# Kernel tuning notes

Measured on AMD Instinct MI355X. Metric: run time of the kernel, lower is better.

## Reference

```python
import jax, jax.numpy as jnp
import numpy as np

B, K, D = 8, 1024, 512
H, DQ, DV = 8, 64, 64


def setup_inputs() -> dict:
    key = jax.random.key(0)
    ks = jax.random.split(key, 11)
    s = 0.02  # param init scale
    return {
        "query": jax.random.normal(ks[0], (B, K, D), jnp.float32),
        "key": jax.random.normal(ks[1], (B, K, D), jnp.float32),
        "value": jax.random.normal(ks[2], (B, K, D), jnp.float32),
        "Wq": jax.random.normal(ks[3], (D, H * DQ), jnp.float32) * s,
        "bq": jax.random.normal(ks[4], (H * DQ,), jnp.float32) * s,
        "Wk": jax.random.normal(ks[5], (D, H * DQ), jnp.float32) * s,
        "bk": jax.random.normal(ks[6], (H * DQ,), jnp.float32) * s,
        "Wv": jax.random.normal(ks[7], (D, H * DV), jnp.float32) * s,
        "bv": jax.random.normal(ks[8], (H * DV,), jnp.float32) * s,
        "Wo": jax.random.normal(ks[9], (H * DV, D), jnp.float32) * s,
        "bo": jax.random.normal(ks[10], (D,), jnp.float32) * s,
    }


def reference(query, key, value, Wq, bq, Wk, bk, Wv, bv, Wo, bo):
    b, k, _ = query.shape
    # Linear projections, split into heads: chunk(h, dim=-1) + cat(dim=0)
    # is equivalent to reshape (b, k, h, d) with head on a separate axis.
    q = (query @ Wq + bq).reshape(b, k, H, DQ)  # b k h dq
    kk = (key @ Wk + bk).reshape(b, k, H, DQ)   # b k h dq
    v = (value @ Wv + bv).reshape(b, k, H, DV)  # b k h dv
    # NOTE: original scales by sqrt(K) (sequence length), not sqrt(dq).
    scale = 1.0 / jnp.sqrt(jnp.asarray(k, q.dtype))
    scores = jnp.einsum("bqhd,bkhd->bhqk", q, kk) * scale
    attn = jax.nn.softmax(scores, axis=-1)
    ctx = jnp.einsum("bhqk,bkhd->bqhd", attn, v).reshape(b, k, H * DV)
    return ctx @ Wo + bo
```

## Files before the change

### kernel.cpp

```cpp
#include <hip/hip_runtime.h>
#include <hip/hip_bf16.h>

#define DEVI __device__ __forceinline__

typedef __attribute__((ext_vector_type(4))) float f32x4;
typedef __attribute__((ext_vector_type(8))) short bf16x8;

static constexpr int BB  = 8;
static constexpr int SEQ = 1024;
static constexpr int DIM = 512;
static constexpr int NH  = 8;
static constexpr int HD  = 64;
static constexpr int M   = BB * SEQ;


DEVI unsigned short f2bf(float x) {
  unsigned int u = __builtin_bit_cast(unsigned int, x);
  u += 0x7fffu + ((u >> 16) & 1u);
  return (unsigned short)(u >> 16);
}

DEVI float fexp2(float x) {
#if __has_builtin(__builtin_amdgcn_exp2f)
  return __builtin_amdgcn_exp2f(x);
#else
  float r; asm("v_exp_f32 %0, %1" : "=v"(r) : "v"(x)); return r;
#endif
}

DEVI void gload_lds16(const unsigned short* g, unsigned short* l) {
  __builtin_amdgcn_global_load_lds(
      (const __attribute__((address_space(1))) void*)g,
      (__attribute__((address_space(3))) void*)l, 16, 0, 0);
}


__global__ __launch_bounds__(256) void cvt3_kernel(const float* __restrict__ a,
                                                   const float* __restrict__ b,
                                                   const float* __restrict__ c,
                                                   unsigned short* __restrict__ oa,
                                                   unsigned short* __restrict__ ob,
                                                   unsigned short* __restrict__ oc) {
  const float* in = (blockIdx.y == 0) ? a : ((blockIdx.y == 1) ? b : c);
  unsigned short* out = (blockIdx.y == 0) ? oa : ((blockIdx.y == 1) ? ob : oc);
  int i = (blockIdx.x * 256 + threadIdx.x) * 4;
  float4 v = *reinterpret_cast<const float4*>(in + i);
  ushort4 o;
  o.x = f2bf(v.x); o.y = f2bf(v.y); o.z = f2bf(v.z); o.w = f2bf(v.w);
  *reinterpret_cast<ushort4*>(out + i) = o;
}


__global__ __launch_bounds__(256) void cvt_t4_kernel(const float* __restrict__ w0,
                                                     const float* __restrict__ w1,
                                                     const float* __restrict__ w2,
                                                     const float* __restrict__ w3,
                                                     unsigned short* __restrict__ o0,
                                                     unsigned short* __restrict__ o1,
                                                     unsigned short* __restrict__ o2,
                                                     unsigned short* __restrict__ o3) {
  const float* in = (blockIdx.z == 0) ? w0 : ((blockIdx.z == 1) ? w1 : ((blockIdx.z == 2) ? w2 : w3));
  unsigned short* out = (blockIdx.z == 0) ? o0 : ((blockIdx.z == 1) ? o1 : ((blockIdx.z == 2) ? o2 : o3));
  __shared__ float tile[32][33];
  int n0 = blockIdx.x * 32, k0 = blockIdx.y * 32;
  int tx = threadIdx.x & 31, ty = threadIdx.x >> 5;
#pragma unroll
  for (int r = 0; r < 32; r += 8)
    tile[ty + r][tx] = in[(size_t)(k0 + ty + r) * DIM + n0 + tx];
  __syncthreads();
#pragma unroll
  for (int r = 0; r < 32; r += 8)
    out[(size_t)(n0 + ty + r) * DIM + k0 + tx] = f2bf(tile[tx][ty + r]);
}


template <bool OUT_F32>
DEVI void gemm_body(const unsigned short* __restrict__ A,
                    const unsigned short* __restrict__ Bt,
                    const float* __restrict__ bias,
                    float gs,
                    void* __restrict__ Cout) {
  __shared__ unsigned short lA[2][128 * 32];
  __shared__ unsigned short lB[2][128 * 32];
  const int tid = threadIdx.x;
  const int lane = tid & 63, wave = tid >> 6;
  const int wr = wave >> 1, wc = wave & 1;
  const int row0 = blockIdx.x * 128, col0 = blockIdx.y * 128;
  const int lr = lane & 15, lg = lane >> 4;

  f32x4 acc[4][4] = {};

  const int s0a = wave * 64;
  const int sA = s0a + lane, rA = sA >> 2, koA = (sA & 3) * 8;
  const int s0b = 256 + wave * 64;
  const int sB = s0b + lane, rB = sB >> 2, koB = (sB & 3) * 8;

#define GEMM_STAGE(buf, k0)                                                        \
  do {                                                                             \
    gload_lds16(A + (size_t)(row0 + rA) * DIM + (k0) + koA, &lA[buf][s0a * 8]);    \
    gload_lds16(Bt + (size_t)(col0 + rA) * DIM + (k0) + koA, &lB[buf][s0a * 8]);   \
    gload_lds16(A + (size_t)(row0 + rB) * DIM + (k0) + koB, &lA[buf][s0b * 8]);    \
    gload_lds16(Bt + (size_t)(col0 + rB) * DIM + (k0) + koB, &lB[buf][s0b * 8]);   \
  } while (0)

  GEMM_STAGE(0, 0);
  __syncthreads();

  constexpr int NT = DIM / 32;
  for (int t = 0; t < NT; ++t) {
    const int cur = t & 1;
    if (t + 1 < NT) GEMM_STAGE(cur ^ 1, (t + 1) * 32);

    bf16x8 af[4], bfr[4];
#pragma unroll
    for (int m = 0; m < 4; ++m)
      af[m] = *reinterpret_cast<const bf16x8*>(&lA[cur][(wr * 64 + m * 16 + lr) * 32 + lg * 8]);
#pragma unroll
    for (int n = 0; n < 4; ++n)
      bfr[n] = *reinterpret_cast<const bf16x8*>(&lB[cur][(wc * 64 + n * 16 + lr) * 32 + lg * 8]);
    __builtin_amdgcn_s_setprio(1);
#pragma unroll
    for (int m = 0; m < 4; ++m)
#pragma unroll
      for (int n = 0; n < 4; ++n)
        acc[m][n] = __builtin_amdgcn_mfma_f32_16x16x32_bf16(af[m], bfr[n], acc[m][n], 0, 0, 0);
    __builtin_amdgcn_s_setprio(0);

    __syncthreads();
  }
#undef GEMM_STAGE

#pragma unroll
  for (int m = 0; m < 4; ++m) {
#pragma unroll
    for (int n = 0; n < 4; ++n) {
      int col = col0 + wc * 64 + n * 16 + lr;
      int r0 = row0 + wr * 64 + m * 16 + lg * 4;
      float bv = bias[col];
#pragma unroll
      for (int j = 0; j < 4; ++j) {
        float val = (acc[m][n][j] + bv) * gs;
        if constexpr (OUT_F32)
          reinterpret_cast<float*>(Cout)[(size_t)(r0 + j) * DIM + col] = val;
        else
          reinterpret_cast<unsigned short*>(Cout)[(size_t)(r0 + j) * DIM + col] = f2bf(val);
      }
    }
  }
}

struct GemmArgs {
  const unsigned short* A;
  const unsigned short* Bt;
  const float* bias;
  unsigned short* C;
  float scale;
};

__global__ __launch_bounds__(256) void gemm_proj(GemmArgs a0, GemmArgs a1, GemmArgs a2) {
  GemmArgs g = (blockIdx.z == 0) ? a0 : ((blockIdx.z == 1) ? a1 : a2);
  gemm_body<false>(g.A, g.Bt, g.bias, g.scale, (void*)g.C);
}

__global__ __launch_bounds__(256) void gemm_out(const unsigned short* __restrict__ A,
                                                const unsigned short* __restrict__ Bt,
                                                const float* __restrict__ bias,
                                                float* __restrict__ C) {
  gemm_body<true>(A, Bt, bias, 1.0f, (void*)C);
}


__global__ __launch_bounds__(256) void transpose_v_kernel(const unsigned short* __restrict__ vbuf,
                                                          unsigned short* __restrict__ vT) {
  __shared__ unsigned short t[64 * 64];
  const int b = blockIdx.z, h = blockIdx.y, s0 = blockIdx.x * 64;
  const int tid = threadIdx.x, lane = tid & 63, wave = tid >> 6;

#pragma unroll
  for (int it = 0; it < 2; ++it) {
    int base = wave * 128 + it * 64;
    int idx = base + lane;
    int r = idx >> 3, c = idx & 7;
    int csrc = c ^ (r >> 3);
    gload_lds16(vbuf + ((size_t)(b * SEQ) + s0 + r) * DIM + h * HD + csrc * 8,
                &t[base * 8]);
  }
  __syncthreads();

#pragma unroll
  for (int it = 0; it < 2; ++it) {
    int o = it * 256 + tid;
    int dv = o >> 3, cs = o & 7;
    bf16x8 v;
#pragma unroll
    for (int k = 0; k < 8; ++k) {
      int s = cs * 8 + k;
      v[k] = (short)t[s * 64 + (((dv >> 3) ^ (s >> 3)) << 3) + (dv & 7)];
    }
    *reinterpret_cast<bf16x8*>(vT + ((size_t)((b * NH + h) * HD) + dv) * SEQ + s0 + cs * 8) = v;
  }
}


__global__ __launch_bounds__(512) void attn_kernel(const unsigned short* __restrict__ qb,
                                                   const unsigned short* __restrict__ kb,
                                                   const unsigned short* __restrict__ vT,
                                                   unsigned short* __restrict__ ctx) {
  __shared__ unsigned short lK[2][64 * 64];
  __shared__ unsigned short lV[2][64 * 64];
  __shared__ unsigned short Pl[8][16 * 72];

  const int b = blockIdx.z, h = blockIdx.y;
  const int tid = threadIdx.x, lane = tid & 63, wave = tid >> 6;
  const int lr = lane & 15, lg = lane >> 4;
  const int q0 = blockIdx.x * 128 + wave * 16;

  const int sr = tid >> 3, sc = (tid & 7) ^ (sr & 7);
  const unsigned short* Kbase = kb + ((size_t)b * SEQ) * DIM + (size_t)h * HD;
  const unsigned short* Vbase = vT + (size_t)(b * NH + h) * HD * SEQ;

  bf16x8 qf0, qf1;
  {
    const unsigned short* qrow = qb + ((size_t)(b * SEQ) + q0 + lr) * DIM + h * HD;
    qf0 = *reinterpret_cast<const bf16x8*>(qrow + lg * 8);
    qf1 = *reinterpret_cast<const bf16x8*>(qrow + 32 + lg * 8);
  }

  float l_r[4] = {0.f, 0.f, 0.f, 0.f};
  f32x4 o_acc[4];
#pragma unroll
  for (int n = 0; n < 4; ++n) o_acc[n] = f32x4{0.f, 0.f, 0.f, 0.f};

  unsigned short* pw = Pl[wave];

  gload_lds16(Kbase + (size_t)sr * DIM + sc * 8, &lK[0][(wave * 64) * 8]);
  gload_lds16(Vbase + (size_t)sr * SEQ + sc * 8, &lV[0][(wave * 64) * 8]);
  __syncthreads();

  for (int t = 0; t < SEQ / 64; ++t) {
    const int cur = t & 1;
    if (t + 1 < SEQ / 64) {
      const int nk = (t + 1) * 64;
      gload_lds16(Kbase + (size_t)(nk + sr) * DIM + sc * 8, &lK[cur ^ 1][(wave * 64) * 8]);
      gload_lds16(Vbase + (size_t)sr * SEQ + nk + sc * 8, &lV[cur ^ 1][(wave * 64) * 8]);
    }

    f32x4 st[4];
    __builtin_amdgcn_s_setprio(1);
#pragma unroll
    for (int kt = 0; kt < 4; ++kt) {
      const int row = kt * 16 + lr;
      const char* rbase = (const char*)&lK[cur][0] + row * 128;
      const int sw = (row & 7) << 4;
      bf16x8 kf0 = *reinterpret_cast<const bf16x8*>(rbase + ((lg * 16) ^ sw));
      bf16x8 kf1 = *reinterpret_cast<const bf16x8*>(rbase + ((64 + lg * 16) ^ sw));
      f32x4 a = {};
      a = __builtin_amdgcn_mfma_f32_16x16x32_bf16(qf0, kf0, a, 0, 0, 0);
      a = __builtin_amdgcn_mfma_f32_16x16x32_bf16(qf1, kf1, a, 0, 0, 0);
      st[kt] = a;
    }
    __builtin_amdgcn_s_setprio(0);

#pragma unroll
    for (int j = 0; j < 4; ++j) {
      float p0 = fexp2(st[0][j]);
      float p1 = fexp2(st[1][j]);
      float p2 = fexp2(st[2][j]);
      float p3 = fexp2(st[3][j]);
      l_r[j] += (p0 + p1) + (p2 + p3);
      const int qrow = (lg * 4 + j) * 72;
      pw[qrow + lr] = f2bf(p0);
      pw[qrow + 16 + lr] = f2bf(p1);
      pw[qrow + 32 + lr] = f2bf(p2);
      pw[qrow + 48 + lr] = f2bf(p3);
    }

#pragma unroll
    for (int c = 0; c < 2; ++c) {
      bf16x8 pf = *reinterpret_cast<const bf16x8*>((const char*)pw + lr * 144 + c * 64 + lg * 16);
      __builtin_amdgcn_s_setprio(1);
#pragma unroll
      for (int n = 0; n < 4; ++n) {
        const int row = n * 16 + lr;
        bf16x8 vf = *reinterpret_cast<const bf16x8*>(
            (const char*)&lV[cur][0] + row * 128 + ((c * 64 + lg * 16) ^ ((row & 7) << 4)));
        o_acc[n] = __builtin_amdgcn_mfma_f32_16x16x32_bf16(pf, vf, o_acc[n], 0, 0, 0);
      }
      __builtin_amdgcn_s_setprio(0);
    }

    __syncthreads();
  }

  float invl[4];
#pragma unroll
  for (int j = 0; j < 4; ++j) {
    float l = l_r[j];
#pragma unroll
    for (int msk = 1; msk < 16; msk <<= 1) l += __shfl_xor(l, msk);
    invl[j] = 1.f / l;
  }
#pragma unroll
  for (int n = 0; n < 4; ++n)
#pragma unroll
    for (int j = 0; j < 4; ++j)
      pw[(lg * 4 + j) * 72 + n * 16 + lr] = f2bf(o_acc[n][j] * invl[j]);

#pragma unroll
  for (int it = 0; it < 2; ++it) {
    int idx = it * 64 + lane;
    int r = idx >> 3, cc = idx & 7;
    bf16x8 v = *reinterpret_cast<const bf16x8*>((const char*)pw + r * 144 + cc * 16);
    *reinterpret_cast<bf16x8*>(ctx + ((size_t)(b * SEQ) + q0 + r) * DIM + h * HD + cc * 8) = v;
  }
}


extern "C" void kernel_launch(void* const* d_in, const int* in_sizes, int n_in,
                              void* d_out, int out_size, void* d_ws, size_t ws_size,
                              hipStream_t stream) {
  const float* query = (const float*)d_in[0];
  const float* key_  = (const float*)d_in[1];
  const float* value = (const float*)d_in[2];
  const float* Wq = (const float*)d_in[3];
  const float* bq = (const float*)d_in[4];
  const float* Wk = (const float*)d_in[5];
  const float* bk = (const float*)d_in[6];
  const float* Wv = (const float*)d_in[7];
  const float* bv = (const float*)d_in[8];
  const float* Wo = (const float*)d_in[9];
  const float* bo = (const float*)d_in[10];
  float* out = (float*)d_out;

  unsigned short* ws = (unsigned short*)d_ws;
  const size_t NM = (size_t)M * DIM;
  const size_t NW = (size_t)DIM * DIM;
  unsigned short* xq   = ws;
  unsigned short* xk   = xq + NM;
  unsigned short* xv   = xk + NM;
  unsigned short* qb   = xv + NM;
  unsigned short* kbuf = qb + NM;
  unsigned short* vbuf = kbuf + NM;
  unsigned short* ctx  = vbuf + NM;
  unsigned short* Wqt  = ctx + NM;
  unsigned short* Wkt  = Wqt + NW;
  unsigned short* Wvt  = Wkt + NW;
  unsigned short* Wot  = Wvt + NW;
  unsigned short* vTb  = xq;

  cvt3_kernel<<<dim3((int)(NM / 1024), 3), 256, 0, stream>>>(query, key_, value, xq, xk, xv);
  cvt_t4_kernel<<<dim3(16, 16, 4), 256, 0, stream>>>(Wq, Wk, Wv, Wo, Wqt, Wkt, Wvt, Wot);

  const float qscale = 0.03125f * 1.4426950408889634f;
  GemmArgs g0{xq, Wqt, bq, qb, qscale}, g1{xk, Wkt, bk, kbuf, 1.0f}, g2{xv, Wvt, bv, vbuf, 1.0f};
  gemm_proj<<<dim3(M / 128, DIM / 128, 3), 256, 0, stream>>>(g0, g1, g2);

  transpose_v_kernel<<<dim3(SEQ / 64, NH, BB), 256, 0, stream>>>(vbuf, vTb);

  attn_kernel<<<dim3(SEQ / 128, NH, BB), 512, 0, stream>>>(qb, kbuf, vTb, ctx);

  gemm_out<<<dim3(M / 128, DIM / 128), 256, 0, stream>>>(ctx, Wot, bo, out);
}
```

Baseline: 87.44 us.

## Fuse fp32-to-bf16 input conversion and V transpose into projection GEMM

The projection GEMM now reads fp32 activations straight from the inputs, converts them to bf16 in registers, and writes them to LDS. This removes the separate conversion kernel and its extra bf16 round trip through global memory. The V projection epilogue stages its tile through LDS and writes V already transposed, so the standalone transpose kernel goes away. In exchange, the A-operand load is now a register-staged, synchronous load with conversion ALU work instead of the async global-to-LDS path, and each A tile moves twice the bytes.

```diff
diff --git a/kernel.cpp b/kernel.cpp
--- a/kernel.cpp
+++ b/kernel.cpp
@@ -34,20 +34,13 @@
       (__attribute__((address_space(3))) void*)l, 16, 0, 0);
 }
 
-
-__global__ __launch_bounds__(256) void cvt3_kernel(const float* __restrict__ a,
-                                                   const float* __restrict__ b,
-                                                   const float* __restrict__ c,
-                                                   unsigned short* __restrict__ oa,
-                                                   unsigned short* __restrict__ ob,
-                                                   unsigned short* __restrict__ oc) {
-  const float* in = (blockIdx.y == 0) ? a : ((blockIdx.y == 1) ? b : c);
-  unsigned short* out = (blockIdx.y == 0) ? oa : ((blockIdx.y == 1) ? ob : oc);
-  int i = (blockIdx.x * 256 + threadIdx.x) * 4;
-  float4 v = *reinterpret_cast<const float4*>(in + i);
-  ushort4 o;
-  o.x = f2bf(v.x); o.y = f2bf(v.y); o.z = f2bf(v.z); o.w = f2bf(v.w);
-  *reinterpret_cast<ushort4*>(out + i) = o;
+DEVI bf16x8 cvt8(float4 a, float4 b) {
+  bf16x8 r;
+  r[0] = (short)f2bf(a.x); r[1] = (short)f2bf(a.y);
+  r[2] = (short)f2bf(a.z); r[3] = (short)f2bf(a.w);
+  r[4] = (short)f2bf(b.x); r[5] = (short)f2bf(b.y);
+  r[6] = (short)f2bf(b.z); r[7] = (short)f2bf(b.w);
+  return r;
 }
 
 
@@ -74,12 +67,151 @@
 }
 
 
-template <bool OUT_F32>
-DEVI void gemm_body(const unsigned short* __restrict__ A,
-                    const unsigned short* __restrict__ Bt,
-                    const float* __restrict__ bias,
-                    float gs,
-                    void* __restrict__ Cout) {
+__global__ __launch_bounds__(256) void gemm_proj(const float* __restrict__ Aq,
+                                                 const float* __restrict__ Ak,
+                                                 const float* __restrict__ Av,
+                                                 const unsigned short* __restrict__ WqT,
+                                                 const unsigned short* __restrict__ WkT,
+                                                 const unsigned short* __restrict__ WvT,
+                                                 const float* __restrict__ bq,
+                                                 const float* __restrict__ bk,
+                                                 const float* __restrict__ bv,
+                                                 unsigned short* __restrict__ qb,
+                                                 unsigned short* __restrict__ kb,
+                                                 unsigned short* __restrict__ vT,
+                                                 float qscale) {
+  __shared__ unsigned short smem[17408];
+  unsigned short* lA = smem;
+  unsigned short* lB = smem + 8192;
+
+  const int z = blockIdx.z;
+  const float* A32 = (z == 0) ? Aq : ((z == 1) ? Ak : Av);
+  const unsigned short* Bt = (z == 0) ? WqT : ((z == 1) ? WkT : WvT);
+  const float* bias = (z == 0) ? bq : ((z == 1) ? bk : bv);
+  const float gs = (z == 0) ? qscale : 1.0f;
+
+  const int tid = threadIdx.x;
+  const int lane = tid & 63, wave = tid >> 6;
+  const int wr = wave >> 1, wc = wave & 1;
+  const int row0 = blockIdx.x * 128, col0 = blockIdx.y * 128;
+  const int lr = lane & 15, lg = lane >> 4;
+
+  f32x4 acc[4][4] = {};
+
+  const int r0s = tid >> 2, k8s = (tid & 3) * 8;
+  const int s0a = wave * 64;
+  const int sAi = s0a + lane, rA = sAi >> 2, koA = (sAi & 3) * 8;
+  const int s0b = 256 + wave * 64;
+  const int sBi = s0b + lane, rB = sBi >> 2, koB = (sBi & 3) * 8;
+
+  float4 ra0, ra1, rb0, rb1;
+
+#define LOADA(k0)                                                              \
+  do {                                                                         \
+    const float* p0 = A32 + (size_t)(row0 + r0s) * DIM + (k0) + k8s;           \
+    ra0 = *reinterpret_cast<const float4*>(p0);                                \
+    ra1 = *reinterpret_cast<const float4*>(p0 + 4);                            \
+    const float* p1 = A32 + (size_t)(row0 + r0s + 64) * DIM + (k0) + k8s;      \
+    rb0 = *reinterpret_cast<const float4*>(p1);                                \
+    rb1 = *reinterpret_cast<const float4*>(p1 + 4);                            \
+  } while (0)
+
+#define WRITEA(buf)                                                            \
+  do {                                                                         \
+    *reinterpret_cast<bf16x8*>(&lA[(buf)*4096 + r0s * 32 + k8s]) = cvt8(ra0, ra1); \
+    *reinterpret_cast<bf16x8*>(&lA[(buf)*4096 + (r0s + 64) * 32 + k8s]) = cvt8(rb0, rb1); \
+  } while (0)
+
+#define STAGEB(buf, k0)                                                        \
+  do {                                                                         \
+    gload_lds16(Bt + (size_t)(col0 + rA) * DIM + (k0) + koA, &lB[(buf)*4096 + s0a * 8]); \
+    gload_lds16(Bt + (size_t)(col0 + rB) * DIM + (k0) + koB, &lB[(buf)*4096 + s0b * 8]); \
+  } while (0)
+
+  LOADA(0);
+  STAGEB(0, 0);
+  WRITEA(0);
+  __syncthreads();
+
+  constexpr int NT = DIM / 32;
+  for (int t = 0; t < NT; ++t) {
+    const int cur = t & 1;
+    if (t + 1 < NT) {
+      LOADA((t + 1) * 32);
+      STAGEB(cur ^ 1, (t + 1) * 32);
+    }
+
+    bf16x8 af[4], bfr[4];
+#pragma unroll
+    for (int m = 0; m < 4; ++m)
+      af[m] = *reinterpret_cast<const bf16x8*>(&lA[cur * 4096 + (wr * 64 + m * 16 + lr) * 32 + lg * 8]);
+#pragma unroll
+    for (int n = 0; n < 4; ++n)
+      bfr[n] = *reinterpret_cast<const bf16x8*>(&lB[cur * 4096 + (wc * 64 + n * 16 + lr) * 32 + lg * 8]);
+    __builtin_amdgcn_s_setprio(1);
+#pragma unroll
+    for (int m = 0; m < 4; ++m)
+#pragma unroll
+      for (int n = 0; n < 4; ++n)
+        acc[m][n] = __builtin_amdgcn_mfma_f32_16x16x32_bf16(af[m], bfr[n], acc[m][n], 0, 0, 0);
+    __builtin_amdgcn_s_setprio(0);
+
+    if (t + 1 < NT) WRITEA(cur ^ 1);
+    __syncthreads();
+  }
+#undef LOADA
+#undef WRITEA
+#undef STAGEB
+
+  if (z < 2) {
+    unsigned short* C = (z == 0) ? qb : kb;
+#pragma unroll
+    for (int m = 0; m < 4; ++m) {
+#pragma unroll
+      for (int n = 0; n < 4; ++n) {
+        int col = col0 + wc * 64 + n * 16 + lr;
+        int r0 = row0 + wr * 64 + m * 16 + lg * 4;
+        float bvv = bias[col];
+#pragma unroll
+        for (int j = 0; j < 4; ++j)
+          C[(size_t)(r0 + j) * DIM + col] = f2bf((acc[m][n][j] + bvv) * gs);
+      }
+    }
+  } else {
+    unsigned short* ldsT = smem;
+#pragma unroll
+    for (int m = 0; m < 4; ++m) {
+#pragma unroll
+      for (int n = 0; n < 4; ++n) {
+        const int col = wc * 64 + n * 16 + lr;
+        const int r0l = wr * 64 + m * 16 + lg * 4;
+        const float bvv = bias[col0 + col];
+        ushort4 pk;
+        pk.x = f2bf(acc[m][n][0] + bvv);
+        pk.y = f2bf(acc[m][n][1] + bvv);
+        pk.z = f2bf(acc[m][n][2] + bvv);
+        pk.w = f2bf(acc[m][n][3] + bvv);
+        *reinterpret_cast<ushort4*>(&ldsT[col * 136 + r0l]) = pk;
+      }
+    }
+    __syncthreads();
+    const int b = row0 >> 10, s_loc0 = row0 & 1023;
+#pragma unroll
+    for (int it = 0; it < 8; ++it) {
+      int idx = it * 256 + tid;
+      int c = idx >> 4, s8 = idx & 15;
+      bf16x8 v = *reinterpret_cast<const bf16x8*>(&ldsT[c * 136 + s8 * 8]);
+      *reinterpret_cast<bf16x8*>(
+          vT + ((size_t)(b * DIM) + col0 + c) * SEQ + s_loc0 + s8 * 8) = v;
+    }
+  }
+}
+
+
+__global__ __launch_bounds__(256) void gemm_out(const unsigned short* __restrict__ A,
+                                                const unsigned short* __restrict__ Bt,
+                                                const float* __restrict__ bias,
+                                                float* __restrict__ C) {
   __shared__ unsigned short lA[2][128 * 32];
   __shared__ unsigned short lB[2][128 * 32];
   const int tid = threadIdx.x;
@@ -138,66 +270,9 @@
       int r0 = row0 + wr * 64 + m * 16 + lg * 4;
       float bv = bias[col];
 #pragma unroll
-      for (int j = 0; j < 4; ++j) {
-        float val = (acc[m][n][j] + bv) * gs;
-        if constexpr (OUT_F32)
-          reinterpret_cast<float*>(Cout)[(size_t)(r0 + j) * DIM + col] = val;
-        else
-          reinterpret_cast<unsigned short*>(Cout)[(size_t)(r0 + j) * DIM + col] = f2bf(val);
-      }
-    }
-  }
-}
-
-struct GemmArgs {
-  const unsigned short* A;
-  const unsigned short* Bt;
-  const float* bias;
-  unsigned short* C;
-  float scale;
-};
-
-__global__ __launch_bounds__(256) void gemm_proj(GemmArgs a0, GemmArgs a1, GemmArgs a2) {
-  GemmArgs g = (blockIdx.z == 0) ? a0 : ((blockIdx.z == 1) ? a1 : a2);
-  gemm_body<false>(g.A, g.Bt, g.bias, g.scale, (void*)g.C);
-}
-
-__global__ __launch_bounds__(256) void gemm_out(const unsigned short* __restrict__ A,
-                                                const unsigned short* __restrict__ Bt,
-                                                const float* __restrict__ bias,
-                                                float* __restrict__ C) {
-  gemm_body<true>(A, Bt, bias, 1.0f, (void*)C);
-}
-
-
-__global__ __launch_bounds__(256) void transpose_v_kernel(const unsigned short* __restrict__ vbuf,
-                                                          unsigned short* __restrict__ vT) {
-  __shared__ unsigned short t[64 * 64];
-  const int b = blockIdx.z, h = blockIdx.y, s0 = blockIdx.x * 64;
-  const int tid = threadIdx.x, lane = tid & 63, wave = tid >> 6;
-
-#pragma unroll
-  for (int it = 0; it < 2; ++it) {
-    int base = wave * 128 + it * 64;
-    int idx = base + lane;
-    int r = idx >> 3, c = idx & 7;
-    int csrc = c ^ (r >> 3);
-    gload_lds16(vbuf + ((size_t)(b * SEQ) + s0 + r) * DIM + h * HD + csrc * 8,
-                &t[base * 8]);
-  }
-  __syncthreads();
-
-#pragma unroll
-  for (int it = 0; it < 2; ++it) {
-    int o = it * 256 + tid;
-    int dv = o >> 3, cs = o & 7;
-    bf16x8 v;
-#pragma unroll
-    for (int k = 0; k < 8; ++k) {
-      int s = cs * 8 + k;
-      v[k] = (short)t[s * 64 + (((dv >> 3) ^ (s >> 3)) << 3) + (dv & 7)];
-    }
-    *reinterpret_cast<bf16x8*>(vT + ((size_t)((b * NH + h) * HD) + dv) * SEQ + s0 + cs * 8) = v;
+      for (int j = 0; j < 4; ++j)
+        C[(size_t)(r0 + j) * DIM + col] = acc[m][n][j] + bv;
+    }
   }
 }
 
@@ -335,27 +410,20 @@
   unsigned short* ws = (unsigned short*)d_ws;
   const size_t NM = (size_t)M * DIM;
   const size_t NW = (size_t)DIM * DIM;
-  unsigned short* xq   = ws;
-  unsigned short* xk   = xq + NM;
-  unsigned short* xv   = xk + NM;
-  unsigned short* qb   = xv + NM;
+  unsigned short* qb   = ws;
   unsigned short* kbuf = qb + NM;
-  unsigned short* vbuf = kbuf + NM;
-  unsigned short* ctx  = vbuf + NM;
+  unsigned short* vTb  = kbuf + NM;
+  unsigned short* ctx  = vTb + NM;
   unsigned short* Wqt  = ctx + NM;
   unsigned short* Wkt  = Wqt + NW;
   unsigned short* Wvt  = Wkt + NW;
   unsigned short* Wot  = Wvt + NW;
-  unsigned short* vTb  = xq;
-
-  cvt3_kernel<<<dim3((int)(NM / 1024), 3), 256, 0, stream>>>(query, key_, value, xq, xk, xv);
+
   cvt_t4_kernel<<<dim3(16, 16, 4), 256, 0, stream>>>(Wq, Wk, Wv, Wo, Wqt, Wkt, Wvt, Wot);
 
   const float qscale = 0.03125f * 1.4426950408889634f;
-  GemmArgs g0{xq, Wqt, bq, qb, qscale}, g1{xk, Wkt, bk, kbuf, 1.0f}, g2{xv, Wvt, bv, vbuf, 1.0f};
-  gemm_proj<<<dim3(M / 128, DIM / 128, 3), 256, 0, stream>>>(g0, g1, g2);
-
-  transpose_v_kernel<<<dim3(SEQ / 64, NH, BB), 256, 0, stream>>>(vbuf, vTb);
+  gemm_proj<<<dim3(M / 128, DIM / 128, 3), 256, 0, stream>>>(
+      query, key_, value, Wqt, Wkt, Wvt, bq, bk, bv, qb, kbuf, vTb, qscale);
 
   attn_kernel<<<dim3(SEQ / 128, NH, BB), 512, 0, stream>>>(qb, kbuf, vTb, ctx);
 
```

Result: no change. 88.29 us (+1.0%).
